# Optimization experiments

Hardware: AMD Instinct MI355X
Metric: run time of the kernel (lower is better)

Reference implementation:

```python
import jax, jax.numpy as jnp
import numpy as np

H = 128
B, N, E = 256, 81, 1620
LN_EPS = 1e-5


def setup_inputs() -> dict:
    key = jax.random.key(0)
    ks = jax.random.split(key, 12)
    s = 0.05
    return {
        "node_features": jax.random.normal(ks[0], (B, N, H), jnp.float32),
        "edge_index": jax.random.randint(ks[1], (2, E), 0, N, jnp.int64),
        "Wm1": jax.random.normal(ks[2], (2 * H, H), jnp.float32) * s,
        "bm1": jnp.zeros((H,), jnp.float32),
        "Wm2": jax.random.normal(ks[3], (H, H), jnp.float32) * s,
        "bm2": jnp.zeros((H,), jnp.float32),
        "Wu1": jax.random.normal(ks[4], (2 * H, H), jnp.float32) * s,
        "bu1": jnp.zeros((H,), jnp.float32),
        "Wu2": jax.random.normal(ks[5], (H, H), jnp.float32) * s,
        "bu2": jnp.zeros((H,), jnp.float32),
        "gamma": jnp.ones((H,), jnp.float32),
        "beta": jnp.zeros((H,), jnp.float32),
    }


def reference(node_features, edge_index, Wm1, bm1, Wm2, bm2, Wu1, bu1, Wu2, bu2, gamma, beta):
    src_idx, tgt_idx = edge_index[0], edge_index[1]
    # Gather: [B, E, H] each (vectorized over batch; original loops in Python)
    src = node_features[:, src_idx]
    tgt = node_features[:, tgt_idx]
    comb = jnp.concatenate([src, tgt], axis=-1)            # [B, E, 2H]
    msgs = jax.nn.relu(comb @ Wm1 + bm1) @ Wm2 + bm2       # [B, E, H]
    # Scatter-mean aggregation at target nodes
    agg = jnp.zeros_like(node_features).at[:, tgt_idx].add(msgs)  # [B, N, H]
    counts = jnp.zeros((N,), node_features.dtype).at[tgt_idx].add(1.0)
    counts = jnp.maximum(counts, 1.0)
    agg = agg / counts[None, :, None]
    # Node update MLP + residual + LayerNorm
    comb2 = jnp.concatenate([node_features, agg], axis=-1)  # [B, N, 2H]
    upd = jax.nn.relu(comb2 @ Wu1 + bu1) @ Wu2 + bu2
    x = node_features + upd
    mu = jnp.mean(x, axis=-1, keepdims=True)
    var = jnp.mean(jnp.square(x - mu), axis=-1, keepdims=True)
    return (x - mu) * jax.lax.rsqrt(var + LN_EPS) * gamma + beta
```

## Files before the change

### kernel.cpp

```cpp
#include <hip/hip_runtime.h>
#include <hip/hip_bf16.h>


#define NN 81
#define HH 128
#define EE 1620
#define NCHK 26
#define MPAD 96
#define WB_BYTES 196608
#define OFFS_OFF (WB_BYTES)
#define CSR_OFF  (OFFS_OFF + 82 * 4)
#define BC_OFF   (CSR_OFF + EE * 4)
#define WS_NEED  (BC_OFF + HH * 4)

typedef __attribute__((ext_vector_type(8))) short bf16x8;
typedef __attribute__((ext_vector_type(8))) unsigned short ushort8v;
typedef __attribute__((ext_vector_type(4))) float f32x4;

__device__ __forceinline__ unsigned short f2b(float f) {
  union { float f; unsigned u; } v; v.f = f;
  unsigned r = v.u + 0x7fffu + ((v.u >> 16) & 1u);
  return (unsigned short)(r >> 16);
}
__device__ __forceinline__ float b2f(unsigned short h) {
  union { unsigned u; float f; } v; v.u = ((unsigned)h) << 16;
  return v.f;
}
__device__ __forceinline__ unsigned f2b2(float x, float y) {
  float2 f; f.x = x; f.y = y;
  union { __hip_bfloat162 h; unsigned u; } v;
  v.h = __float22bfloat162_rn(f);
  return v.u;
}
__device__ __forceinline__ unsigned swzu(int r, int laneb) {
  return ((unsigned)(r * 256 + laneb)) ^ ((unsigned)((r & 7) << 4));
}

__global__ __launch_bounds__(1024)
void setup_kernel(const float* __restrict__ Wm1, const float* __restrict__ Wm2,
                  const float* __restrict__ Wu1, const float* __restrict__ Wu2,
                  const float* __restrict__ bm2, const int* __restrict__ eidx,
                  char* __restrict__ ws) {
  __shared__ __align__(16) char arena[81920];
  const int tid = threadIdx.x;

  if (blockIdx.x < 8) {
    const int gid = blockIdx.x * 1024 + tid;
    const int lane = gid & 63;
    const int t = gid >> 6;
    const int ks = t & 3, nt = (t >> 2) & 7, mat = t >> 5;
    const float* src;
    int slot;
    if (mat == 0)      { src = Wm1;           slot = 0; }
    else if (mat == 1) { src = Wm1 + HH * HH; slot = 1; }
    else if (mat == 2) { src = Wu1;           slot = 3; }
    else               { src = Wu2;           slot = 5; }
    const int c = nt * 16 + (lane & 15);
    const int k0 = ks * 32 + (lane >> 4) * 8;
    bf16x8 pv;
#pragma unroll
    for (int j = 0; j < 8; ++j) pv[j] = (short)f2b(src[(k0 + j) * HH + c]);
    *(bf16x8*)((unsigned short*)ws + (size_t)slot * 16384 + (((nt * 4 + ks) * 64) + lane) * 8) = pv;
    return;
  }

  if (blockIdx.x == 8) {
    int* srcE  = (int*)arena;
    int* tgtE  = srcE + EE;
    int* rankS = tgtE + EE;
    int* cntC  = rankS + EE;
    int* tot   = cntC + NCHK * NN;
    int* scanS = tot + NN;
    int* wsumS = scanS + 128;
    int* offsS = wsumS + 2;
    for (int i = tid; i < NCHK * NN; i += 1024) cntC[i] = 0;
    for (int i = tid; i < 2 * EE; i += 1024) srcE[i] = eidx[i];
    __syncthreads();
    const int lane = tid & 63, wv = tid >> 6;
    for (int c = wv; c < NCHK; c += 16) {
      const int e = c * 64 + lane;
      const bool ok = (e < EE);
      const int t = ok ? tgtE[e] : -1;
      unsigned long long mymask = 0;
#pragma unroll
      for (int i = 0; i < 64; ++i) {
        const int ti = __shfl(t, i);
        const unsigned long long bal = __ballot(t == ti);
        if (i == lane) mymask = bal;
      }
      if (ok) {
        const int rank = __popcll(mymask & ((1ull << lane) - 1ull));
        rankS[e] = rank;
        if (rank == 0) cntC[c * NN + t] = __popcll(mymask);
      }
    }
    __syncthreads();
    if (tid < NN) {
      int s = 0;
#pragma unroll
      for (int c = 0; c < NCHK; ++c) s += cntC[c * NN + tid];
      tot[tid] = s;
    }
    __syncthreads();
    if (tid < 128) {
      const int l = tid & 63, w = tid >> 6;
      int inc = (tid < NN) ? tot[tid] : 0;
#pragma unroll
      for (int d = 1; d < 64; d <<= 1) {
        int u = __shfl_up(inc, d);
        if (l >= d) inc += u;
      }
      scanS[tid] = inc;
      if (l == 63) wsumS[w] = inc;
    }
    __syncthreads();
    if (tid < 128) {
      const int w = tid >> 6;
      const int inc = scanS[tid] + (w ? wsumS[0] : 0);
      if (tid < NN) offsS[tid] = inc - tot[tid];
      if (tid == NN - 1) offsS[NN] = inc;
    }
    __syncthreads();
    if (tid < NN) {
      int run = offsS[tid];
#pragma unroll
      for (int c = 0; c < NCHK; ++c) {
        const int tmp = cntC[c * NN + tid];
        cntC[c * NN + tid] = run;
        run += tmp;
      }
    }
    __syncthreads();
    int* wofs = (int*)(ws + OFFS_OFF);
    int* wcsr = (int*)(ws + CSR_OFF);
    for (int i = tid; i <= NN; i += 1024) wofs[i] = offsS[i];
    for (int e = tid; e < EE; e += 1024) {
      const int t = tgtE[e];
      wcsr[cntC[(e >> 6) * NN + t] + rankS[e]] = srcE[e];
    }
    return;
  }

  {
    const int bs = blockIdx.x - 9;
    float* WuL = (float*)arena;
    float* WmL = WuL + HH * HH;
    const float* Wu1b = Wu1 + HH * HH;
    float4* WuL4 = (float4*)WuL;
    const float4* src4 = (const float4*)Wu1b;
    for (int i = tid; i < HH * HH / 4; i += 1024) WuL4[i] = src4[i];
    const float4* wm4 = (const float4*)(Wm2 + bs * 32 * HH);
    float4* WmL4 = (float4*)WmL;
    if (tid < 32 * HH / 4) WmL4[tid] = wm4[tid];
    __syncthreads();
    const int kk = tid >> 5;
    const int k  = bs * 32 + kk;
    const int cg = tid & 31;
    f32x4 acc = (f32x4)0.f;
    for (int j = 0; j < HH; ++j) {
      const float a = WmL[kk * HH + j];
      const float4 w = WuL4[j * 32 + cg];
      acc[0] += a * w.x; acc[1] += a * w.y; acc[2] += a * w.z; acc[3] += a * w.w;
    }
    unsigned short* dst = (unsigned short*)ws;
#pragma unroll
    for (int q = 0; q < 4; ++q) {
      const int c = cg * 4 + q;
      const int nt = c >> 4;
      const int l = (((k & 31) >> 3) << 4) | (c & 15);
      dst[(size_t)2 * 16384 + (((nt * 4 + bs) * 64) + l) * 8 + (k & 7)] = f2b(acc[q]);
    }
    if (bs == 0 && tid < HH) {
      float s = 0.f;
      for (int j = 0; j < HH; ++j) s += bm2[j] * WuL[j * HH + tid];
      ((float*)(ws + BC_OFF))[tid] = s;
    }
  }
}

__device__ __forceinline__ void gemm3x1(const unsigned short* Ab, const unsigned short* Wp,
                                        int lane, int mt0, int nt0, f32x4 acc[3]) {
  bf16x8 Bf[4];
#pragma unroll
  for (int ks = 0; ks < 4; ++ks)
    Bf[ks] = *(const bf16x8*)(Wp + ((nt0 * 4 + ks) * 64 + lane) * 8);
  const int rl = lane & 15;
  const int kb = (lane >> 4) * 16;
  const unsigned swz = (unsigned)((rl & 7) << 4);
#pragma unroll
  for (int ks = 0; ks < 4; ++ks)
#pragma unroll
    for (int mm = 0; mm < 3; ++mm) {
      const int r = (mt0 + mm) * 16 + rl;
      const unsigned byte = (unsigned)(r * 256) + (((unsigned)(ks * 64 + kb)) ^ swz);
      bf16x8 a = *(const bf16x8*)((const char*)Ab + byte);
      acc[mm] = __builtin_amdgcn_mfma_f32_16x16x32_bf16(a, Bf[ks], acc[mm], 0, 0, 0);
    }
}

__device__ __forceinline__ void gemm3x1x2(const unsigned short* Ab,
                                          const unsigned short* Wp0, const unsigned short* Wp1,
                                          int lane, int mt0, int nt0,
                                          f32x4 acc0[3], f32x4 acc1[3]) {
  bf16x8 B0[4], B1[4];
#pragma unroll
  for (int ks = 0; ks < 4; ++ks) {
    B0[ks] = *(const bf16x8*)(Wp0 + ((nt0 * 4 + ks) * 64 + lane) * 8);
    B1[ks] = *(const bf16x8*)(Wp1 + ((nt0 * 4 + ks) * 64 + lane) * 8);
  }
  const int rl = lane & 15;
  const int kb = (lane >> 4) * 16;
  const unsigned swz = (unsigned)((rl & 7) << 4);
#pragma unroll
  for (int ks = 0; ks < 4; ++ks)
#pragma unroll
    for (int mm = 0; mm < 3; ++mm) {
      const int r = (mt0 + mm) * 16 + rl;
      const unsigned byte = (unsigned)(r * 256) + (((unsigned)(ks * 64 + kb)) ^ swz);
      bf16x8 a = *(const bf16x8*)((const char*)Ab + byte);
      acc0[mm] = __builtin_amdgcn_mfma_f32_16x16x32_bf16(a, B0[ks], acc0[mm], 0, 0, 0);
      acc1[mm] = __builtin_amdgcn_mfma_f32_16x16x32_bf16(a, B1[ks], acc1[mm], 0, 0, 0);
    }
}

__device__ __forceinline__ void gemm3x1_2A(const unsigned short* A0, const unsigned short* A1,
                                           const unsigned short* Wp0, const unsigned short* Wp1,
                                           int lane, int mt0, int nt0,
                                           f32x4 acc0[3], f32x4 acc1[3]) {
  bf16x8 B0[4], B1[4];
#pragma unroll
  for (int ks = 0; ks < 4; ++ks) {
    B0[ks] = *(const bf16x8*)(Wp0 + ((nt0 * 4 + ks) * 64 + lane) * 8);
    B1[ks] = *(const bf16x8*)(Wp1 + ((nt0 * 4 + ks) * 64 + lane) * 8);
  }
  const int rl = lane & 15;
  const int kb = (lane >> 4) * 16;
  const unsigned swz = (unsigned)((rl & 7) << 4);
#pragma unroll
  for (int ks = 0; ks < 4; ++ks)
#pragma unroll
    for (int mm = 0; mm < 3; ++mm) {
      const int r = (mt0 + mm) * 16 + rl;
      const unsigned byte = (unsigned)(r * 256) + (((unsigned)(ks * 64 + kb)) ^ swz);
      bf16x8 a0 = *(const bf16x8*)((const char*)A0 + byte);
      acc0[mm] = __builtin_amdgcn_mfma_f32_16x16x32_bf16(a0, B0[ks], acc0[mm], 0, 0, 0);
      bf16x8 a1 = *(const bf16x8*)((const char*)A1 + byte);
      acc1[mm] = __builtin_amdgcn_mfma_f32_16x16x32_bf16(a1, B1[ks], acc1[mm], 0, 0, 0);
    }
}

__global__ __launch_bounds__(1024, 4)
void mpnn_mfma4_kernel(const float* __restrict__ node,
                       const float* __restrict__ bm1,
                       const float* __restrict__ bu1, const float* __restrict__ bu2,
                       const float* __restrict__ gamma_, const float* __restrict__ beta_,
                       const char* __restrict__ ws,
                       float* __restrict__ out) {
  __shared__ float X[NN][HH];
  __shared__ unsigned short Xb[MPAD * HH];
  __shared__ unsigned short bufP[MPAD * HH];
  __shared__ unsigned short bufQ[MPAD * HH];
  __shared__ int   csrL[EE];
  __shared__ int   offsL[NN + 1];
  __shared__ float bias[6][HH];

  const int tid  = threadIdx.x;
  const int lane = tid & 63;
  const int wave = tid >> 6;
  const int b    = blockIdx.x;

  const unsigned short* wpk = (const unsigned short*)ws;
  const int* wofs = (const int*)(ws + OFFS_OFF);
  const int* wcsr = (const int*)(ws + CSR_OFF);
  const float* wbc = (const float*)(ws + BC_OFF);

  {
    const float4* nf4 = (const float4*)(node + (size_t)b * NN * HH);
    const int i2 = tid + 2048;
    const bool has2 = (i2 < NN * HH / 4);
    float4 v0 = nf4[tid];
    float4 v1 = nf4[tid + 1024];
    float4 v2 = has2 ? nf4[i2] : make_float4(0.f, 0.f, 0.f, 0.f);
#pragma unroll
    for (int k = 0; k < 3; ++k) {
      const int i = tid + k * 1024;
      if (k == 2 && !has2) break;
      const float4 v = (k == 0) ? v0 : (k == 1) ? v1 : v2;
      const int r = i >> 5, c = (i & 31) * 4;
      *(float4*)&X[r][c] = v;
      unsigned pk0 = f2b2(v.x, v.y), pk1 = f2b2(v.z, v.w);
      uint2 pv; pv.x = pk0; pv.y = pk1;
      *(uint2*)((char*)Xb + swzu(r, c * 2)) = pv;
    }
    if (tid < (MPAD - NN) * 16) {
      const int r = NN + tid / 16, m = tid % 16;
      ushort8v z = {0,0,0,0,0,0,0,0};
      *(ushort8v*)((char*)Xb + swzu(r, m * 16)) = z;
    }
    for (int i = tid; i < EE; i += 1024) csrL[i] = wcsr[i];
    if (tid < NN + 1) offsL[tid] = wofs[tid];
    if (tid < HH) {
      bias[0][tid] = bm1[tid];  bias[1][tid] = wbc[tid];
      bias[2][tid] = bu1[tid];  bias[3][tid] = bu2[tid];
      bias[4][tid] = gamma_[tid]; bias[5][tid] = beta_[tid];
    }
  }
  __syncthreads();

  const int nt0 = wave & 7;
  const int mt0 = 3 * (wave >> 3);
  const int erow = (lane >> 4) * 4;
  const int ecol = lane & 15;

  {
    f32x4 accP[3], accQ[3];
#pragma unroll
    for (int mm = 0; mm < 3; ++mm) { accP[mm] = (f32x4)0.f; accQ[mm] = (f32x4)0.f; }
    gemm3x1x2(Xb, wpk, wpk + 16384, lane, mt0, nt0, accP, accQ);
#pragma unroll
    for (int mm = 0; mm < 3; ++mm)
#pragma unroll
      for (int rg = 0; rg < 4; ++rg) {
        const int R = (mt0 + mm) * 16 + erow + rg;
        const int C = nt0 * 16 + ecol;
        const unsigned byte = swzu(R, C * 2);
        const bool ok = (R < NN);
        *(unsigned short*)((char*)bufP + byte) = ok ? f2b(accP[mm][rg]) : (unsigned short)0;
        *(unsigned short*)((char*)bufQ + byte) = ok ? f2b(accQ[mm][rg] + bias[0][C]) : (unsigned short)0;
      }
  }
  __syncthreads();

  {
    const int lb = lane * 4;
    for (int t = wave; t < NN; t += 16) {
      const unsigned qbyte = swzu(t, lb);
      const unsigned pq = *(const unsigned*)((const char*)bufQ + qbyte);
      const float q0 = b2f((unsigned short)(pq & 0xffff));
      const float q1 = b2f((unsigned short)(pq >> 16));
      float h0 = 0.f, h1 = 0.f, g0 = 0.f, g1 = 0.f;
      int e = offsL[t];
      const int o1 = offsL[t + 1];
      for (; e + 4 <= o1; e += 4) {
        const int s0 = csrL[e], s1 = csrL[e + 1], s2 = csrL[e + 2], s3 = csrL[e + 3];
        const unsigned p0 = *(const unsigned*)((const char*)bufP + swzu(s0, lb));
        const unsigned p1 = *(const unsigned*)((const char*)bufP + swzu(s1, lb));
        const unsigned p2 = *(const unsigned*)((const char*)bufP + swzu(s2, lb));
        const unsigned p3 = *(const unsigned*)((const char*)bufP + swzu(s3, lb));
        h0 += fmaxf(b2f((unsigned short)(p0 & 0xffff)) + q0, 0.f);
        h1 += fmaxf(b2f((unsigned short)(p0 >> 16))    + q1, 0.f);
        g0 += fmaxf(b2f((unsigned short)(p1 & 0xffff)) + q0, 0.f);
        g1 += fmaxf(b2f((unsigned short)(p1 >> 16))    + q1, 0.f);
        h0 += fmaxf(b2f((unsigned short)(p2 & 0xffff)) + q0, 0.f);
        h1 += fmaxf(b2f((unsigned short)(p2 >> 16))    + q1, 0.f);
        g0 += fmaxf(b2f((unsigned short)(p3 & 0xffff)) + q0, 0.f);
        g1 += fmaxf(b2f((unsigned short)(p3 >> 16))    + q1, 0.f);
      }
      for (; e < o1; ++e) {
        const int s = csrL[e];
        const unsigned pp = *(const unsigned*)((const char*)bufP + swzu(s, lb));
        h0 += fmaxf(b2f((unsigned short)(pp & 0xffff)) + q0, 0.f);
        h1 += fmaxf(b2f((unsigned short)(pp >> 16))    + q1, 0.f);
      }
      h0 += g0; h1 += g1;
      const unsigned hv = (unsigned)f2b(h0) | ((unsigned)f2b(h1) << 16);
      *(unsigned*)((char*)bufQ + qbyte) = hv;
    }
  }
  __syncthreads();

  {
    f32x4 accT[3], accU[3];
#pragma unroll
    for (int mm = 0; mm < 3; ++mm) { accT[mm] = (f32x4)0.f; accU[mm] = (f32x4)0.f; }
    gemm3x1_2A(bufQ, Xb, wpk + 2 * 16384, wpk + 3 * 16384, lane, mt0, nt0, accT, accU);
#pragma unroll
    for (int mm = 0; mm < 3; ++mm)
#pragma unroll
      for (int rg = 0; rg < 4; ++rg) {
        const int R = (mt0 + mm) * 16 + erow + rg;
        const int C = nt0 * 16 + ecol;
        float v = 0.f;
        if (R < NN) {
          const int dg = offsL[R + 1] - offsL[R];
          const float inv = (dg > 0) ? 1.f / (float)dg : 1.f;
          const float sf  = (dg > 0) ? 1.f : 0.f;
          v = fmaxf(accU[mm][rg] + accT[mm][rg] * inv + sf * bias[1][C] + bias[2][C], 0.f);
        }
        *(unsigned short*)((char*)bufP + swzu(R, C * 2)) = f2b(v);
      }
  }
  __syncthreads();

  {
    f32x4 acc[3];
#pragma unroll
    for (int mm = 0; mm < 3; ++mm) acc[mm] = (f32x4)0.f;
    gemm3x1(bufP, wpk + 5 * 16384, lane, mt0, nt0, acc);
#pragma unroll
    for (int mm = 0; mm < 3; ++mm)
#pragma unroll
      for (int rg = 0; rg < 4; ++rg) {
        const int R = (mt0 + mm) * 16 + erow + rg;
        const int C = nt0 * 16 + ecol;
        if (R < NN) X[R][C] += acc[mm][rg] + bias[3][C];
      }
  }
  __syncthreads();

  for (int r = wave; r < NN; r += 16) {
    const float x0 = X[r][lane], x1 = X[r][lane + 64];
    float s = x0 + x1;
#pragma unroll
    for (int off = 32; off; off >>= 1) s += __shfl_xor(s, off);
    const float mu = s * (1.f / 128.f);
    const float d0 = x0 - mu, d1 = x1 - mu;
    float v = d0 * d0 + d1 * d1;
#pragma unroll
    for (int off = 32; off; off >>= 1) v += __shfl_xor(v, off);
    const float rstd = rsqrtf(v * (1.f / 128.f) + 1e-5f);
    const size_t o = ((size_t)b * NN + r) * HH;
    out[o + lane]      = d0 * rstd * bias[4][lane]      + bias[5][lane];
    out[o + lane + 64] = d1 * rstd * bias[4][lane + 64] + bias[5][lane + 64];
  }
}

__device__ __forceinline__ void gemm_acc_f32(const float (*A)[HH], const float* __restrict__ Wg,
                                             int c, int row0, int nr, float (&acc)[41]) {
  float w[8];
#pragma unroll
  for (int j = 0; j < 8; ++j) w[j] = Wg[j * HH + c];
  for (int k0 = 0; k0 < HH; k0 += 8) {
    float wn[8];
    if (k0 + 8 < HH) {
#pragma unroll
      for (int j = 0; j < 8; ++j) wn[j] = Wg[(k0 + 8 + j) * HH + c];
    }
#pragma unroll
    for (int i = 0; i < 41; ++i) {
      if (i < nr) {
        const float4 a0 = *(const float4*)&A[row0 + i][k0];
        const float4 a1 = *(const float4*)&A[row0 + i][k0 + 4];
        acc[i] += a0.x * w[0] + a0.y * w[1] + a0.z * w[2] + a0.w * w[3]
                + a1.x * w[4] + a1.y * w[5] + a1.z * w[6] + a1.w * w[7];
      }
    }
#pragma unroll
    for (int j = 0; j < 8; ++j) w[j] = wn[j];
  }
}

__global__ __launch_bounds__(256, 1)
void mpnn_fused_kernel(const float* __restrict__ node, const int* __restrict__ eidx,
                       const float* __restrict__ Wm1, const float* __restrict__ bm1,
                       const float* __restrict__ Wm2, const float* __restrict__ bm2,
                       const float* __restrict__ Wu1, const float* __restrict__ bu1,
                       const float* __restrict__ Wu2, const float* __restrict__ bu2,
                       const float* __restrict__ gamma_, const float* __restrict__ beta_,
                       float* __restrict__ out) {
  __shared__ float X[NN][HH];
  __shared__ float Pb[NN][HH];
  __shared__ float Qb[NN][HH];
  __shared__ int   edg[2 * EE];
  __shared__ int   csr[EE];
  __shared__ int   offs[NN + 1];
  __shared__ int   cnt3[3][NN];
  __shared__ int   base3[3][NN];
  __shared__ float biases[6][HH];

  const int tid  = threadIdx.x;
  const int lane = tid & 63;
  const int wave = tid >> 6;
  const int b    = blockIdx.x;

  {
    const float4* nf4 = (const float4*)(node + (size_t)b * NN * HH);
    float4* X4 = (float4*)&X[0][0];
    for (int i = tid; i < NN * HH / 4; i += 256) X4[i] = nf4[i];
    for (int i = tid; i < 2 * EE; i += 256) edg[i] = eidx[i];
    if (tid < HH) {
      biases[0][tid] = bm1[tid]; biases[1][tid] = bm2[tid];
      biases[2][tid] = bu1[tid]; biases[3][tid] = bu2[tid];
      biases[4][tid] = gamma_[tid]; biases[5][tid] = beta_[tid];
    }
  }
  __syncthreads();
  if (tid < 3 * NN) {
    const int t = tid % NN, ch = tid / NN;
    const int e0 = ch * 540, e1 = e0 + 540;
    int cnt = 0;
    for (int e = e0; e < e1; ++e) cnt += (edg[EE + e] == t);
    cnt3[ch][t] = cnt;
  }
  __syncthreads();
  if (tid == 0) {
    int run = 0;
    for (int t = 0; t < NN; ++t) {
      offs[t] = run;
      base3[0][t] = run;
      base3[1][t] = base3[0][t] + cnt3[0][t];
      base3[2][t] = base3[1][t] + cnt3[1][t];
      run = base3[2][t] + cnt3[2][t];
    }
    offs[NN] = run;
  }
  __syncthreads();
  if (tid < 3 * NN) {
    const int t = tid % NN, ch = tid / NN;
    const int e0 = ch * 540, e1 = e0 + 540;
    int pos = base3[ch][t];
    for (int e = e0; e < e1; ++e)
      if (edg[EE + e] == t) csr[pos++] = edg[e];
  }
  __syncthreads();

  const int c    = ((wave & 1) << 6) | lane;
  const int row0 = (wave >> 1) ? 41 : 0;
  const int nr   = (wave >> 1) ? 40 : 41;

  {
    float acc[41];
#pragma unroll
    for (int i = 0; i < 41; ++i) acc[i] = 0.f;
    gemm_acc_f32(X, Wm1, c, row0, nr, acc);
#pragma unroll
    for (int i = 0; i < 41; ++i) if (i < nr) Pb[row0 + i][c] = acc[i];
  }
  {
    float acc[41];
#pragma unroll
    for (int i = 0; i < 41; ++i) acc[i] = 0.f;
    gemm_acc_f32(X, Wm1 + HH * HH, c, row0, nr, acc);
#pragma unroll
    for (int i = 0; i < 41; ++i) if (i < nr) Qb[row0 + i][c] = acc[i];
  }
  __syncthreads();

  for (int t = wave; t < NN; t += 4) {
    const int o0 = offs[t], o1 = offs[t + 1];
    const float q0 = Qb[t][lane]      + biases[0][lane];
    const float q1 = Qb[t][lane + 64] + biases[0][lane + 64];
    float h0 = 0.f, h1 = 0.f;
    for (int e = o0; e < o1; ++e) {
      const int s = csr[e];
      h0 += fmaxf(Pb[s][lane]      + q0, 0.f);
      h1 += fmaxf(Pb[s][lane + 64] + q1, 0.f);
    }
    Qb[t][lane]      = h0;
    Qb[t][lane + 64] = h1;
  }
  __syncthreads();

  {
    float acc[41];
#pragma unroll
    for (int i = 0; i < 41; ++i) acc[i] = 0.f;
    gemm_acc_f32(Qb, Wm2, c, row0, nr, acc);
#pragma unroll
    for (int i = 0; i < 41; ++i) if (i < nr) {
      const int r = row0 + i;
      const float d = (float)(offs[r + 1] - offs[r]);
      Pb[r][c] = (acc[i] + d * biases[1][c]) * (1.f / fmaxf(d, 1.f));
    }
  }
  __syncthreads();

  {
    float acc[41];
#pragma unroll
    for (int i = 0; i < 41; ++i) acc[i] = 0.f;
    gemm_acc_f32(X,  Wu1,           c, row0, nr, acc);
    gemm_acc_f32(Pb, Wu1 + HH * HH, c, row0, nr, acc);
#pragma unroll
    for (int i = 0; i < 41; ++i) if (i < nr)
      Qb[row0 + i][c] = fmaxf(acc[i] + biases[2][c], 0.f);
  }
  __syncthreads();

  {
    float acc[41];
#pragma unroll
    for (int i = 0; i < 41; ++i) acc[i] = 0.f;
    gemm_acc_f32(Qb, Wu2, c, row0, nr, acc);
#pragma unroll
    for (int i = 0; i < 41; ++i) if (i < nr) {
      const int r = row0 + i;
      X[r][c] = X[r][c] + acc[i] + biases[3][c];
    }
  }
  __syncthreads();

  for (int r = wave; r < NN; r += 4) {
    const float x0 = X[r][lane], x1 = X[r][lane + 64];
    float s = x0 + x1;
#pragma unroll
    for (int off = 32; off; off >>= 1) s += __shfl_xor(s, off);
    const float mu = s * (1.f / 128.f);
    const float d0 = x0 - mu, d1 = x1 - mu;
    float v = d0 * d0 + d1 * d1;
#pragma unroll
    for (int off = 32; off; off >>= 1) v += __shfl_xor(v, off);
    const float rstd = rsqrtf(v * (1.f / 128.f) + 1e-5f);
    const size_t o = ((size_t)b * NN + r) * HH;
    out[o + lane]      = d0 * rstd * biases[4][lane]      + biases[5][lane];
    out[o + lane + 64] = d1 * rstd * biases[4][lane + 64] + biases[5][lane + 64];
  }
}

extern "C" void kernel_launch(void* const* d_in, const int* in_sizes, int n_in,
                              void* d_out, int out_size, void* d_ws, size_t ws_size,
                              hipStream_t stream) {
  (void)in_sizes; (void)n_in; (void)out_size;
  const float* node  = (const float*)d_in[0];
  const int*   eidx  = (const int*)  d_in[1];
  const float* Wm1   = (const float*)d_in[2];
  const float* bm1   = (const float*)d_in[3];
  const float* Wm2   = (const float*)d_in[4];
  const float* bm2   = (const float*)d_in[5];
  const float* Wu1   = (const float*)d_in[6];
  const float* bu1   = (const float*)d_in[7];
  const float* Wu2   = (const float*)d_in[8];
  const float* bu2   = (const float*)d_in[9];
  const float* gamma_= (const float*)d_in[10];
  const float* beta_ = (const float*)d_in[11];
  float* outp = (float*)d_out;

  if (ws_size >= (size_t)WS_NEED) {
    char* ws = (char*)d_ws;
    hipLaunchKernelGGL(setup_kernel, dim3(13), dim3(1024), 0, stream,
                       Wm1, Wm2, Wu1, Wu2, bm2, eidx, ws);
    hipLaunchKernelGGL(mpnn_mfma4_kernel, dim3(256), dim3(1024), 0, stream,
                       node, bm1, bu1, bu2, gamma_, beta_, ws, outp);
  } else {
    hipLaunchKernelGGL(mpnn_fused_kernel, dim3(256), dim3(256), 0, stream,
                       node, eidx, Wm1, bm1, Wm2, bm2, Wu1, bu1, Wu2, bu2,
                       gamma_, beta_, outp);
  }
}
```

Baseline: 41.78 us.

## Split each graph across two blocks by target-node halves

```diff
diff --git a/kernel.cpp b/kernel.cpp
--- a/kernel.cpp
+++ b/kernel.cpp
@@ -12,6 +12,14 @@
 #define CSR_OFF  (OFFS_OFF + 82 * 4)
 #define BC_OFF   (CSR_OFF + EE * 4)
 #define WS_NEED  (BC_OFF + HH * 4)
+
+#define XB_OFF   0
+#define BP_OFF   24576
+#define BQ_OFF   49152
+#define CSRL_OFF 61440
+#define OFFH_OFF 67920
+#define BIAS_OFF 68128
+#define L_BYTES  71232
 
 typedef __attribute__((ext_vector_type(8))) short bf16x8;
 typedef __attribute__((ext_vector_type(8))) unsigned short ushort8v;
@@ -178,127 +186,99 @@
   }
 }
 
-__device__ __forceinline__ void gemm3x1(const unsigned short* Ab, const unsigned short* Wp,
-                                        int lane, int mt0, int nt0, f32x4 acc[3]) {
-  bf16x8 Bf[4];
+__device__ __forceinline__ void loadB(const unsigned short* Wp, int nt0, int lane,
+                                      bf16x8 (&Bf)[4]) {
 #pragma unroll
   for (int ks = 0; ks < 4; ++ks)
     Bf[ks] = *(const bf16x8*)(Wp + ((nt0 * 4 + ks) * 64 + lane) * 8);
+}
+
+template <int MT>
+__device__ __forceinline__ void gemmNx1(const char* Ab, int rowbase,
+                                        const bf16x8 (&Bf)[4], int lane,
+                                        f32x4 (&acc)[MT]) {
   const int rl = lane & 15;
   const int kb = (lane >> 4) * 16;
   const unsigned swz = (unsigned)((rl & 7) << 4);
 #pragma unroll
   for (int ks = 0; ks < 4; ++ks)
 #pragma unroll
-    for (int mm = 0; mm < 3; ++mm) {
-      const int r = (mt0 + mm) * 16 + rl;
+    for (int mm = 0; mm < MT; ++mm) {
+      const int r = rowbase + mm * 16 + rl;
       const unsigned byte = (unsigned)(r * 256) + (((unsigned)(ks * 64 + kb)) ^ swz);
-      bf16x8 a = *(const bf16x8*)((const char*)Ab + byte);
+      bf16x8 a = *(const bf16x8*)(Ab + byte);
       acc[mm] = __builtin_amdgcn_mfma_f32_16x16x32_bf16(a, Bf[ks], acc[mm], 0, 0, 0);
     }
 }
 
-__device__ __forceinline__ void gemm3x1x2(const unsigned short* Ab,
-                                          const unsigned short* Wp0, const unsigned short* Wp1,
-                                          int lane, int mt0, int nt0,
-                                          f32x4 acc0[3], f32x4 acc1[3]) {
-  bf16x8 B0[4], B1[4];
-#pragma unroll
-  for (int ks = 0; ks < 4; ++ks) {
-    B0[ks] = *(const bf16x8*)(Wp0 + ((nt0 * 4 + ks) * 64 + lane) * 8);
-    B1[ks] = *(const bf16x8*)(Wp1 + ((nt0 * 4 + ks) * 64 + lane) * 8);
-  }
-  const int rl = lane & 15;
-  const int kb = (lane >> 4) * 16;
-  const unsigned swz = (unsigned)((rl & 7) << 4);
-#pragma unroll
-  for (int ks = 0; ks < 4; ++ks)
-#pragma unroll
-    for (int mm = 0; mm < 3; ++mm) {
-      const int r = (mt0 + mm) * 16 + rl;
-      const unsigned byte = (unsigned)(r * 256) + (((unsigned)(ks * 64 + kb)) ^ swz);
-      bf16x8 a = *(const bf16x8*)((const char*)Ab + byte);
-      acc0[mm] = __builtin_amdgcn_mfma_f32_16x16x32_bf16(a, B0[ks], acc0[mm], 0, 0, 0);
-      acc1[mm] = __builtin_amdgcn_mfma_f32_16x16x32_bf16(a, B1[ks], acc1[mm], 0, 0, 0);
-    }
-}
-
-__device__ __forceinline__ void gemm3x1_2A(const unsigned short* A0, const unsigned short* A1,
-                                           const unsigned short* Wp0, const unsigned short* Wp1,
-                                           int lane, int mt0, int nt0,
-                                           f32x4 acc0[3], f32x4 acc1[3]) {
-  bf16x8 B0[4], B1[4];
-#pragma unroll
-  for (int ks = 0; ks < 4; ++ks) {
-    B0[ks] = *(const bf16x8*)(Wp0 + ((nt0 * 4 + ks) * 64 + lane) * 8);
-    B1[ks] = *(const bf16x8*)(Wp1 + ((nt0 * 4 + ks) * 64 + lane) * 8);
-  }
-  const int rl = lane & 15;
-  const int kb = (lane >> 4) * 16;
-  const unsigned swz = (unsigned)((rl & 7) << 4);
-#pragma unroll
-  for (int ks = 0; ks < 4; ++ks)
-#pragma unroll
-    for (int mm = 0; mm < 3; ++mm) {
-      const int r = (mt0 + mm) * 16 + rl;
-      const unsigned byte = (unsigned)(r * 256) + (((unsigned)(ks * 64 + kb)) ^ swz);
-      bf16x8 a0 = *(const bf16x8*)((const char*)A0 + byte);
-      acc0[mm] = __builtin_amdgcn_mfma_f32_16x16x32_bf16(a0, B0[ks], acc0[mm], 0, 0, 0);
-      bf16x8 a1 = *(const bf16x8*)((const char*)A1 + byte);
-      acc1[mm] = __builtin_amdgcn_mfma_f32_16x16x32_bf16(a1, B1[ks], acc1[mm], 0, 0, 0);
-    }
-}
-
-__global__ __launch_bounds__(1024, 4)
-void mpnn_mfma4_kernel(const float* __restrict__ node,
-                       const float* __restrict__ bm1,
-                       const float* __restrict__ bu1, const float* __restrict__ bu2,
-                       const float* __restrict__ gamma_, const float* __restrict__ beta_,
-                       const char* __restrict__ ws,
-                       float* __restrict__ out) {
-  __shared__ float X[NN][HH];
-  __shared__ unsigned short Xb[MPAD * HH];
-  __shared__ unsigned short bufP[MPAD * HH];
-  __shared__ unsigned short bufQ[MPAD * HH];
-  __shared__ int   csrL[EE];
-  __shared__ int   offsL[NN + 1];
-  __shared__ float bias[6][HH];
+__global__ __launch_bounds__(512, 4)
+void mpnn_half_kernel(const float* __restrict__ node,
+                      const float* __restrict__ bm1,
+                      const float* __restrict__ bu1, const float* __restrict__ bu2,
+                      const float* __restrict__ gamma_, const float* __restrict__ beta_,
+                      const char* __restrict__ ws,
+                      float* __restrict__ out) {
+  __shared__ __align__(16) char L[L_BYTES];
+  char* Xb   = L + XB_OFF;
+  char* bufP = L + BP_OFF;
+  char* bufQ = L + BQ_OFF;
+  int*  csrL = (int*)(L + CSRL_OFF);
+  int*  offsH= (int*)(L + OFFH_OFF);
+  float (*bias)[HH] = (float(*)[HH])(L + BIAS_OFF);
+  float* xout = (float*)(L + BP_OFF);
 
   const int tid  = threadIdx.x;
   const int lane = tid & 63;
   const int wave = tid >> 6;
-  const int b    = blockIdx.x;
+  const int b    = blockIdx.x & 255;
+  const int half = blockIdx.x >> 8;
+  const int t0   = half * 48;
+  const int tcnt = half ? (NN - 48) : 48;
+  const int rbase = half * 48;
 
   const unsigned short* wpk = (const unsigned short*)ws;
   const int* wofs = (const int*)(ws + OFFS_OFF);
   const int* wcsr = (const int*)(ws + CSR_OFF);
   const float* wbc = (const float*)(ws + BC_OFF);
 
+  const int nt0 = wave;
+  const int erow = (lane >> 4) * 4;
+  const int ecol = lane & 15;
+
+  bf16x8 BA0[4], BA1[4];
+  loadB(wpk, nt0, lane, BA0);
+  loadB(wpk + 16384, nt0, lane, BA1);
+
   {
     const float4* nf4 = (const float4*)(node + (size_t)b * NN * HH);
-    const int i2 = tid + 2048;
-    const bool has2 = (i2 < NN * HH / 4);
-    float4 v0 = nf4[tid];
-    float4 v1 = nf4[tid + 1024];
-    float4 v2 = has2 ? nf4[i2] : make_float4(0.f, 0.f, 0.f, 0.f);
-#pragma unroll
-    for (int k = 0; k < 3; ++k) {
-      const int i = tid + k * 1024;
-      if (k == 2 && !has2) break;
-      const float4 v = (k == 0) ? v0 : (k == 1) ? v1 : v2;
+    float4 v[5];
+#pragma unroll
+    for (int k = 0; k < 5; ++k) v[k] = nf4[tid + k * 512];
+    const bool tail = (tid < 2592 - 2560);
+    float4 v5;
+    if (tail) v5 = nf4[tid + 2560];
+#pragma unroll
+    for (int k = 0; k < 5; ++k) {
+      const int i = tid + k * 512;
       const int r = i >> 5, c = (i & 31) * 4;
-      *(float4*)&X[r][c] = v;
-      unsigned pk0 = f2b2(v.x, v.y), pk1 = f2b2(v.z, v.w);
-      uint2 pv; pv.x = pk0; pv.y = pk1;
-      *(uint2*)((char*)Xb + swzu(r, c * 2)) = pv;
+      uint2 pv; pv.x = f2b2(v[k].x, v[k].y); pv.y = f2b2(v[k].z, v[k].w);
+      *(uint2*)(Xb + swzu(r, c * 2)) = pv;
+    }
+    if (tail) {
+      const int i = tid + 2560;
+      const int r = i >> 5, c = (i & 31) * 4;
+      uint2 pv; pv.x = f2b2(v5.x, v5.y); pv.y = f2b2(v5.z, v5.w);
+      *(uint2*)(Xb + swzu(r, c * 2)) = pv;
     }
     if (tid < (MPAD - NN) * 16) {
       const int r = NN + tid / 16, m = tid % 16;
       ushort8v z = {0,0,0,0,0,0,0,0};
-      *(ushort8v*)((char*)Xb + swzu(r, m * 16)) = z;
-    }
-    for (int i = tid; i < EE; i += 1024) csrL[i] = wcsr[i];
-    if (tid < NN + 1) offsL[tid] = wofs[tid];
+      *(ushort8v*)(Xb + swzu(r, m * 16)) = z;
+    }
+    const int e0 = wofs[t0];
+    if (tid <= tcnt) offsH[tid] = wofs[t0 + tid] - e0;
+    const int ecnt = wofs[t0 + tcnt] - e0;
+    for (int i = tid; i < ecnt; i += 512) csrL[i] = wcsr[e0 + i];
     if (tid < HH) {
       bias[0][tid] = bm1[tid];  bias[1][tid] = wbc[tid];
       bias[2][tid] = bu1[tid];  bias[3][tid] = bu2[tid];
@@ -307,46 +287,50 @@
   }
   __syncthreads();
 
-  const int nt0 = wave & 7;
-  const int mt0 = 3 * (wave >> 3);
-  const int erow = (lane >> 4) * 4;
-  const int ecol = lane & 15;
-
-  {
-    f32x4 accP[3], accQ[3];
-#pragma unroll
-    for (int mm = 0; mm < 3; ++mm) { accP[mm] = (f32x4)0.f; accQ[mm] = (f32x4)0.f; }
-    gemm3x1x2(Xb, wpk, wpk + 16384, lane, mt0, nt0, accP, accQ);
+  {
+    f32x4 accP[6], accQ[3];
+#pragma unroll
+    for (int mm = 0; mm < 6; ++mm) accP[mm] = (f32x4)0.f;
+#pragma unroll
+    for (int mm = 0; mm < 3; ++mm) accQ[mm] = (f32x4)0.f;
+    gemmNx1<6>(Xb, 0, BA0, lane, accP);
+    gemmNx1<3>(Xb, rbase, BA1, lane, accQ);
+    const int C = nt0 * 16 + ecol;
+#pragma unroll
+    for (int mm = 0; mm < 6; ++mm)
+#pragma unroll
+      for (int rg = 0; rg < 4; ++rg) {
+        const int R = mm * 16 + erow + rg;
+        *(unsigned short*)(bufP + swzu(R, C * 2)) = f2b(accP[mm][rg]);
+      }
 #pragma unroll
     for (int mm = 0; mm < 3; ++mm)
 #pragma unroll
       for (int rg = 0; rg < 4; ++rg) {
-        const int R = (mt0 + mm) * 16 + erow + rg;
-        const int C = nt0 * 16 + ecol;
-        const unsigned byte = swzu(R, C * 2);
-        const bool ok = (R < NN);
-        *(unsigned short*)((char*)bufP + byte) = ok ? f2b(accP[mm][rg]) : (unsigned short)0;
-        *(unsigned short*)((char*)bufQ + byte) = ok ? f2b(accQ[mm][rg] + bias[0][C]) : (unsigned short)0;
+        const int lr = mm * 16 + erow + rg;
+        const bool ok = (rbase + lr < NN);
+        *(unsigned short*)(bufQ + swzu(lr, C * 2)) =
+            ok ? f2b(accQ[mm][rg] + bias[0][C]) : (unsigned short)0;
       }
   }
   __syncthreads();
 
   {
     const int lb = lane * 4;
-    for (int t = wave; t < NN; t += 16) {
-      const unsigned qbyte = swzu(t, lb);
-      const unsigned pq = *(const unsigned*)((const char*)bufQ + qbyte);
+    for (int tl = wave; tl < tcnt; tl += 8) {
+      const unsigned qbyte = swzu(tl, lb);
+      const unsigned pq = *(const unsigned*)(bufQ + qbyte);
       const float q0 = b2f((unsigned short)(pq & 0xffff));
       const float q1 = b2f((unsigned short)(pq >> 16));
       float h0 = 0.f, h1 = 0.f, g0 = 0.f, g1 = 0.f;
-      int e = offsL[t];
-      const int o1 = offsL[t + 1];
+      int e = offsH[tl];
+      const int o1 = offsH[tl + 1];
       for (; e + 4 <= o1; e += 4) {
         const int s0 = csrL[e], s1 = csrL[e + 1], s2 = csrL[e + 2], s3 = csrL[e + 3];
-        const unsigned p0 = *(const unsigned*)((const char*)bufP + swzu(s0, lb));
-        const unsigned p1 = *(const unsigned*)((const char*)bufP + swzu(s1, lb));
-        const unsigned p2 = *(const unsigned*)((const char*)bufP + swzu(s2, lb));
-        const unsigned p3 = *(const unsigned*)((const char*)bufP + swzu(s3, lb));
+        const unsigned p0 = *(const unsigned*)(bufP + swzu(s0, lb));
+        const unsigned p1 = *(const unsigned*)(bufP + swzu(s1, lb));
+        const unsigned p2 = *(const unsigned*)(bufP + swzu(s2, lb));
+        const unsigned p3 = *(const unsigned*)(bufP + swzu(s3, lb));
         h0 += fmaxf(b2f((unsigned short)(p0 & 0xffff)) + q0, 0.f);
         h1 += fmaxf(b2f((unsigned short)(p0 >> 16))    + q1, 0.f);
         g0 += fmaxf(b2f((unsigned short)(p1 & 0xffff)) + q0, 0.f);
@@ -358,70 +342,101 @@
       }
       for (; e < o1; ++e) {
         const int s = csrL[e];
-        const unsigned pp = *(const unsigned*)((const char*)bufP + swzu(s, lb));
+        const unsigned pp = *(const unsigned*)(bufP + swzu(s, lb));
         h0 += fmaxf(b2f((unsigned short)(pp & 0xffff)) + q0, 0.f);
         h1 += fmaxf(b2f((unsigned short)(pp >> 16))    + q1, 0.f);
       }
       h0 += g0; h1 += g1;
       const unsigned hv = (unsigned)f2b(h0) | ((unsigned)f2b(h1) << 16);
-      *(unsigned*)((char*)bufQ + qbyte) = hv;
-    }
-  }
-  __syncthreads();
-
-  {
+      *(unsigned*)(bufQ + qbyte) = hv;
+    }
+  }
+  __syncthreads();
+
+  {
+    bf16x8 BW[4], BU[4];
+    loadB(wpk + 2 * 16384, nt0, lane, BW);
+    loadB(wpk + 3 * 16384, nt0, lane, BU);
     f32x4 accT[3], accU[3];
 #pragma unroll
     for (int mm = 0; mm < 3; ++mm) { accT[mm] = (f32x4)0.f; accU[mm] = (f32x4)0.f; }
-    gemm3x1_2A(bufQ, Xb, wpk + 2 * 16384, wpk + 3 * 16384, lane, mt0, nt0, accT, accU);
+    gemmNx1<3>(bufQ, 0, BW, lane, accT);
+    gemmNx1<3>(Xb, rbase, BU, lane, accU);
+    const int C = nt0 * 16 + ecol;
 #pragma unroll
     for (int mm = 0; mm < 3; ++mm)
 #pragma unroll
       for (int rg = 0; rg < 4; ++rg) {
-        const int R = (mt0 + mm) * 16 + erow + rg;
-        const int C = nt0 * 16 + ecol;
+        const int lr = mm * 16 + erow + rg;
         float v = 0.f;
-        if (R < NN) {
-          const int dg = offsL[R + 1] - offsL[R];
+        if (lr < tcnt) {
+          const int dg = offsH[lr + 1] - offsH[lr];
           const float inv = (dg > 0) ? 1.f / (float)dg : 1.f;
           const float sf  = (dg > 0) ? 1.f : 0.f;
           v = fmaxf(accU[mm][rg] + accT[mm][rg] * inv + sf * bias[1][C] + bias[2][C], 0.f);
         }
-        *(unsigned short*)((char*)bufP + swzu(R, C * 2)) = f2b(v);
-      }
-  }
-  __syncthreads();
-
-  {
-    f32x4 acc[3];
-#pragma unroll
-    for (int mm = 0; mm < 3; ++mm) acc[mm] = (f32x4)0.f;
-    gemm3x1(bufP, wpk + 5 * 16384, lane, mt0, nt0, acc);
+        *(unsigned short*)(bufP + swzu(lr, C * 2)) = f2b(v);
+      }
+  }
+  __syncthreads();
+
+  {
+    bf16x8 BD[4];
+    loadB(wpk + 5 * 16384, nt0, lane, BD);
+    f32x4 accD[3];
+#pragma unroll
+    for (int mm = 0; mm < 3; ++mm) accD[mm] = (f32x4)0.f;
+    gemmNx1<3>(bufP, 0, BD, lane, accD);
+    __syncthreads();
+    const float* nodeB = node + (size_t)b * NN * HH;
+    const int C = nt0 * 16 + ecol;
 #pragma unroll
     for (int mm = 0; mm < 3; ++mm)
 #pragma unroll
       for (int rg = 0; rg < 4; ++rg) {
-        const int R = (mt0 + mm) * 16 + erow + rg;
-        const int C = nt0 * 16 + ecol;
-        if (R < NN) X[R][C] += acc[mm][rg] + bias[3][C];
-      }
-  }
-  __syncthreads();
-
-  for (int r = wave; r < NN; r += 16) {
-    const float x0 = X[r][lane], x1 = X[r][lane + 64];
-    float s = x0 + x1;
-#pragma unroll
-    for (int off = 32; off; off >>= 1) s += __shfl_xor(s, off);
-    const float mu = s * (1.f / 128.f);
-    const float d0 = x0 - mu, d1 = x1 - mu;
-    float v = d0 * d0 + d1 * d1;
-#pragma unroll
-    for (int off = 32; off; off >>= 1) v += __shfl_xor(v, off);
-    const float rstd = rsqrtf(v * (1.f / 128.f) + 1e-5f);
-    const size_t o = ((size_t)b * NN + r) * HH;
-    out[o + lane]      = d0 * rstd * bias[4][lane]      + bias[5][lane];
-    out[o + lane + 64] = d1 * rstd * bias[4][lane + 64] + bias[5][lane + 64];
+        const int lr = mm * 16 + erow + rg;
+        if (lr < tcnt) {
+          const int R = t0 + lr;
+          const float resid = nodeB[R * HH + C];
+          xout[lr * HH + C] = resid + accD[mm][rg] + bias[3][C];
+        }
+      }
+  }
+  __syncthreads();
+
+  {
+    float x0[6], x1[6], mu[6], rstd[6];
+#pragma unroll
+    for (int k = 0; k < 6; ++k) {
+      const int lr = wave + 8 * k;
+      const int rr = (lr < tcnt) ? lr : 0;
+      x0[k] = xout[rr * HH + lane]; x1[k] = xout[rr * HH + lane + 64];
+    }
+#pragma unroll
+    for (int k = 0; k < 6; ++k) {
+      float s = x0[k] + x1[k];
+#pragma unroll
+      for (int off = 32; off; off >>= 1) s += __shfl_xor(s, off);
+      mu[k] = s * (1.f / 128.f);
+    }
+#pragma unroll
+    for (int k = 0; k < 6; ++k) {
+      const float d0 = x0[k] - mu[k], d1 = x1[k] - mu[k];
+      float v = d0 * d0 + d1 * d1;
+#pragma unroll
+      for (int off = 32; off; off >>= 1) v += __shfl_xor(v, off);
+      rstd[k] = rsqrtf(v * (1.f / 128.f) + 1e-5f);
+    }
+#pragma unroll
+    for (int k = 0; k < 6; ++k) {
+      const int lr = wave + 8 * k;
+      if (lr < tcnt) {
+        const float d0 = x0[k] - mu[k], d1 = x1[k] - mu[k];
+        const size_t o = ((size_t)b * NN + (t0 + lr)) * HH;
+        out[o + lane]      = d0 * rstd[k] * bias[4][lane]      + bias[5][lane];
+        out[o + lane + 64] = d1 * rstd[k] * bias[4][lane + 64] + bias[5][lane + 64];
+      }
+    }
   }
 }
 
@@ -629,7 +644,7 @@
     char* ws = (char*)d_ws;
     hipLaunchKernelGGL(setup_kernel, dim3(13), dim3(1024), 0, stream,
                        Wm1, Wm2, Wu1, Wu2, bm2, eidx, ws);
-    hipLaunchKernelGGL(mpnn_mfma4_kernel, dim3(256), dim3(1024), 0, stream,
+    hipLaunchKernelGGL(mpnn_half_kernel, dim3(512), dim3(512), 0, stream,
                        node, bm1, bu1, bu2, gamma_, beta_, ws, outp);
   } else {
     hipLaunchKernelGGL(mpnn_fused_kernel, dim3(256), dim3(256), 0, stream,
```

After: 44.54 us. +6.6%, slower.
